# Optimization experiments

Measured on AMD Instinct MI355X. Metric: run time of the kernel, lower is better.

The kernel has to match this reference:

```python
import math
import jax, jax.numpy as jnp
import numpy as np

RMS_EPS = 1.1920929e-07  # torch.finfo(float32).eps used by F.rms_norm default

def _rms_norm(x):
    return x * jax.lax.rsqrt(jnp.mean(jnp.square(x), axis=-1, keepdims=True) + RMS_EPS)

def _rope(x, cos, sin):
    # x: [B,T,H,D]; cos/sin: [T, D//2]
    d = x.shape[-1] // 2
    x1, x2 = x[..., :d], x[..., d:]
    c = cos[None, :, None, :]
    s = sin[None, :, None, :]
    return jnp.concatenate([x1 * c + x2 * s, -x1 * s + x2 * c], axis=-1).astype(x.dtype)

def setup_inputs():
    key = jax.random.key(0)
    ks = jax.random.split(key, 8)
    B, T, C, H, D = 2, 2048, 2048, 16, 128
    x = jax.random.normal(ks[0], (B, T, C), dtype=jnp.float32)
    # real RoPE tables for [T, D//2]
    half = D // 2
    inv_freq = 1.0 / (10000.0 ** (np.arange(half, dtype=np.float32) / half))
    ang = np.outer(np.arange(T, dtype=np.float32), inv_freq)
    cos = jnp.asarray(np.cos(ang), dtype=jnp.float32)
    sin = jnp.asarray(np.sin(ang), dtype=jnp.float32)
    s = 0.02
    Wq = jax.random.normal(ks[1], (C, H * D), dtype=jnp.float32) * s
    Wk = jax.random.normal(ks[2], (C, H * D), dtype=jnp.float32) * s
    Wv = jax.random.normal(ks[3], (C, H * D), dtype=jnp.float32) * s
    Wo = jax.random.normal(ks[4], (C, C), dtype=jnp.float32) * s
    fgate_w = jax.random.normal(ks[5], (C, H), dtype=jnp.float32) * s
    fgate_b = jnp.zeros((H,), dtype=jnp.float32)
    weight_lambda = jax.random.normal(ks[6], (C, H), dtype=jnp.float32) * s
    return dict(x=x, cos=cos, sin=sin, Wq=Wq, Wk=Wk, Wv=Wv, Wo=Wo,
                fgate_w=fgate_w, fgate_b=fgate_b, weight_lambda=weight_lambda,
                window_size=1024)

def reference(x, cos, sin, Wq, Wk, Wv, Wo, fgate_w, fgate_b, weight_lambda, window_size):
    B, T, C = x.shape
    H = fgate_w.shape[1]
    D = Wq.shape[1] // H
    sm_scale = 1.0 / math.sqrt(D)
    # QKV projections (bias=False)
    q = (x @ Wq).reshape(B, T, H, D)
    k = (x @ Wk).reshape(B, T, H, D)
    v = (x @ Wv).reshape(B, T, H, D)
    # RoPE then parameter-free RMSNorm on q,k
    q = _rms_norm(_rope(q, cos, sin))
    k = _rms_norm(_rope(k, cos, sin))
    # [B,H,T,D]
    q = q.transpose(0, 2, 1, 3)
    k = k.transpose(0, 2, 1, 3)
    v = v.transpose(0, 2, 1, 3)
    # forgetting gate: log f_t per (B,H,T)
    lam = jax.nn.elu((x @ weight_lambda).astype(jnp.float32)) + 1.0          # [B,T,H]
    logit = (x @ fgate_w + fgate_b) * lam                                    # [B,T,H]
    log_fgate = (jax.nn.log_sigmoid(logit) / (lam + 0.001)).transpose(0, 2, 1)  # [B,H,T]
    cumF = jnp.cumsum(log_fgate, axis=-1)                                    # [B,H,T]
    # forgetting flash attention, dense reference: bias_ij = cumF_i - cumF_j
    scores = jnp.einsum('bhqd,bhkd->bhqk', q.astype(jnp.float32), k.astype(jnp.float32)) * sm_scale
    scores = scores + cumF[..., :, None] - cumF[..., None, :]
    i = jnp.arange(T)[:, None]
    j = jnp.arange(T)[None, :]
    allowed = (j <= i) & (i - j < window_size)  # causal + sliding window
    scores = jnp.where(allowed, scores, -jnp.inf)
    attn = jax.nn.softmax(scores, axis=-1)
    y = jnp.einsum('bhqk,bhkd->bhqd', attn, v.astype(jnp.float32)).astype(x.dtype)
    y = y.transpose(0, 2, 1, 3).reshape(B, T, C)
    return y @ Wo
```

## Files before the change

### kernel.cpp

```cpp
#include <hip/hip_runtime.h>
#include <hip/hip_bf16.h>
#include <stdint.h>

#define T_SEQ 2048
#define CDIM  2048
#define NHEAD 16
#define DHEAD 128
#define BT    4096
#define BHT   32
#define NQKV  6144

typedef __bf16 bf16x8_t __attribute__((ext_vector_type(8)));
typedef float  f32x4_t  __attribute__((ext_vector_type(4)));
typedef unsigned short u16x8_t __attribute__((ext_vector_type(8)));
typedef unsigned short u16x4_t __attribute__((ext_vector_type(4)));

__device__ __forceinline__ unsigned short f2bf(float f){
  unsigned int u = __float_as_uint(f);
  u += 0x7fffu + ((u >> 16) & 1u);
  return (unsigned short)(u >> 16);
}
__device__ __forceinline__ float bf2f(unsigned short h){
  return __uint_as_float(((unsigned int)h) << 16);
}
__device__ __forceinline__ unsigned ldsaddr(const void* p){
  return (unsigned)(size_t)(const __attribute__((address_space(3))) void*)p;
}
__device__ __forceinline__ u16x4_t tr16(unsigned a){
  u16x4_t r;
  asm volatile("ds_read_b64_tr_b16 %0, %1" : "=v"(r) : "v"(a));
  return r;
}

__global__ __launch_bounds__(256) void transpose_all(const float* __restrict__ Wq,
    const float* __restrict__ Wk, const float* __restrict__ Wv,
    const float* __restrict__ Wo, unsigned short* __restrict__ WqkvT,
    unsigned short* __restrict__ WoT){
  __shared__ float tile[32][33];
  const int z = blockIdx.z;
  const float* W = (z==0)?Wq:(z==1)?Wk:(z==2)?Wv:Wo;
  unsigned short* Wt = (z<3) ? (WqkvT + (size_t)z*4194304) : WoT;
  int n0 = blockIdx.x*32, k0 = blockIdx.y*32;
  int tx = threadIdx.x, ty = threadIdx.y;
  #pragma unroll
  for (int i=0;i<32;i+=8)
    tile[ty+i][tx] = W[(size_t)(k0+ty+i)*CDIM + n0 + tx];
  __syncthreads();
  #pragma unroll
  for (int i=0;i<32;i+=8)
    Wt[(size_t)(n0+ty+i)*CDIM + k0 + tx] = f2bf(tile[tx][ty+i]);
}

__global__ __launch_bounds__(256) void build_wgt(const float* __restrict__ fgw,
                                                 const float* __restrict__ wlam,
                                                 float* __restrict__ WgT){
  int idx = blockIdx.x*256 + threadIdx.x;
  int c = idx >> 11, k = idx & 2047;
  const float* W = (c < 16) ? fgw : wlam;
  WgT[idx] = W[k*16 + (c & 15)];
}

#define V3_SYNC() do{ __builtin_amdgcn_sched_barrier(0); \
  __builtin_amdgcn_s_barrier(); \
  asm volatile("s_waitcnt lgkmcnt(0)" ::: "memory"); \
  __builtin_amdgcn_sched_barrier(0); }while(0)

#define V3_TAIL() do{ asm volatile("s_waitcnt vmcnt(3)" ::: "memory"); \
  __builtin_amdgcn_sched_barrier(0); \
  __builtin_amdgcn_s_barrier(); }while(0)

#define V3_MFMA() do{ __builtin_amdgcn_s_setprio(1); \
  _Pragma("unroll") for (int mi=0;mi<4;mi++) \
  _Pragma("unroll") for (int ni=0;ni<4;ni++) \
    acc[mi][ni] = __builtin_amdgcn_mfma_f32_16x16x32_bf16(af[mi], bfr[ni], acc[mi][ni],0,0,0); \
  __builtin_amdgcn_s_setprio(0); }while(0)

#define V3_PHASE(BUF, TIDX) do{ \
  readA(BUF); readB(BUF); \
  { int ts_ = (TIDX)+2; if (ts_ > ntm1) ts_ = ntm1; stage(((BUF)+2)%3, ts_); } \
  V3_SYNC(); V3_MFMA(); V3_TAIL(); }while(0)

template<int MODE>
__global__ __launch_bounds__(512, 2) void gemm_v3(const unsigned short* __restrict__ A,
                                                  const unsigned short* __restrict__ Bt,
                                                  void* __restrict__ Cout,
                                                  int M, int N, int K){
  extern __shared__ unsigned short lds[];
  const int nx = N >> 8;
  const int Mt = M >> 7;
  const int bid = blockIdx.x;
  const int c8 = bid & 7, w = bid >> 3;
  const int mh = Mt >> 1;
  const int mt = (c8 & 1)*mh + (w % mh);
  const int ntc = (c8 >> 1)*(nx >> 2) + (w / mh);
  const int m0 = mt << 7, n0 = ntc << 8;
  const int tid = threadIdx.x, lane = tid & 63, wv = tid >> 6;
  const int wm = wv >> 2, wn = wv & 3;
  const int g = lane >> 4, qi = lane & 15;
  const int ntm1 = (K >> 5) - 1;

  f32x4_t acc[4][4] = {};
  bf16x8_t af[4], bfr[4];

  int goffA, goffB[2];
  { int s = tid; int row = s >> 2; int lg = (s & 3) ^ ((row >> 1) & 3);
    goffA = row*K + lg*8; }
  #pragma unroll
  for (int j=0;j<2;j++){
    int s = j*512 + tid;
    int row = s >> 2;
    int lg = (s & 3) ^ ((row >> 1) & 3);
    goffB[j] = row*K + lg*8;
  }

  auto stage = [&](int buf, int kt){
    const unsigned short* srcA = A + (size_t)m0*K + kt*32;
    const unsigned short* srcB = Bt + (size_t)n0*K + kt*32;
    unsigned short* base = lds + buf*12288;
    __builtin_amdgcn_global_load_lds(
        (const __attribute__((address_space(1))) void*)(srcA + goffA),
        (__attribute__((address_space(3))) void*)(base + tid*8), 16, 0, 0);
    #pragma unroll
    for (int j=0;j<2;j++)
      __builtin_amdgcn_global_load_lds(
        (const __attribute__((address_space(1))) void*)(srcB + goffB[j]),
        (__attribute__((address_space(3))) void*)(base + 4096 + (j*512 + tid)*8), 16, 0, 0);
  };
  auto readA = [&](int buf){
    const unsigned short* base = lds + buf*12288;
    #pragma unroll
    for (int mi=0;mi<4;mi++){
      int row = wm*64 + mi*16 + qi;
      int gs = g ^ ((row >> 1) & 3);
      af[mi] = *reinterpret_cast<const bf16x8_t*>(base + (row*4 + gs)*8);
    }
  };
  auto readB = [&](int buf){
    const unsigned short* base = lds + buf*12288 + 4096;
    #pragma unroll
    for (int ni=0;ni<4;ni++){
      int row = wn*64 + ni*16 + qi;
      int gs = g ^ ((row >> 1) & 3);
      bfr[ni] = *reinterpret_cast<const bf16x8_t*>(base + (row*4 + gs)*8);
    }
  };

  stage(0,0); stage(1,1);
  asm volatile("s_waitcnt vmcnt(3)" ::: "memory");
  __builtin_amdgcn_sched_barrier(0);
  __builtin_amdgcn_s_barrier();

  for (int it=0; it<21; ++it){
    const int t3 = it*3;
    V3_PHASE(0, t3+0);
    V3_PHASE(1, t3+1);
    V3_PHASE(2, t3+2);
  }
  V3_PHASE(0, 63);
  asm volatile("s_waitcnt vmcnt(0)" ::: "memory");

  #pragma unroll
  for (int mi=0;mi<4;mi++){
    #pragma unroll
    for (int ni=0;ni<4;ni++){
      #pragma unroll
      for (int r=0;r<4;r++){
        int mm = m0 + wm*64 + mi*16 + 4*g + r;
        int nn = n0 + wn*64 + ni*16 + qi;
        float v = acc[mi][ni][r];
        if (MODE == 2){
          ((float*)Cout)[(size_t)mm*N + nn] = v;
        } else {
          int bb2 = mm >> 11, t = mm & (T_SEQ-1);
          int which = nn >> 11;
          int hh = (nn >> 7) & 15, d = nn & (DHEAD-1);
          ((unsigned short*)Cout)[(size_t)which*8388608 +
              (((size_t)bb2*NHEAD + hh)*T_SEQ + t)*DHEAD + d] = f2bf(v);
        }
      }
    }
  }
}

#define GROWS 4
__global__ __launch_bounds__(256) void gates_kernel(const float* __restrict__ x,
    const float* __restrict__ WgT, const float* __restrict__ fgb,
    float* __restrict__ lfg, unsigned short* __restrict__ xb){
  __shared__ float xs[GROWS*2048];
  __shared__ float part[GROWS*32*8];
  const int r0 = blockIdx.x*GROWS;
  const int tid = threadIdx.x;
  const float* xp = x + (size_t)r0*CDIM;
  #pragma unroll
  for (int i=0;i<GROWS*2048/(256*4); i++){
    int e = (i*256+tid)*4;
    *(float4*)(xs+e) = *(const float4*)(xp+e);
  }
  __syncthreads();
  #pragma unroll
  for (int i=0;i<GROWS*2048/(256*8); i++){
    int e = (i*256+tid)*8;
    u16x8_t ob;
    #pragma unroll
    for (int j=0;j<8;j++) ob[j] = f2bf(xs[e+j]);
    *reinterpret_cast<u16x8_t*>(xb + (size_t)r0*CDIM + e) = ob;
  }
  const int c = tid & 31, kseg = tid >> 5;
  const float* wp = WgT + c*2048 + kseg*256;
  const float* xq = xs + kseg*256;
  f32x4_t acc[GROWS] = {};
  for (int kk=0; kk<64; kk++){
    f32x4_t wv = *(const f32x4_t*)(wp + kk*4);
    #pragma unroll
    for (int r=0;r<GROWS;r++){
      f32x4_t xv = *(const f32x4_t*)(xq + r*2048 + kk*4);
      acc[r] += xv*wv;
    }
  }
  #pragma unroll
  for (int r=0;r<GROWS;r++)
    part[(r*32 + c)*8 + kseg] = acc[r][0]+acc[r][1]+acc[r][2]+acc[r][3];
  __syncthreads();
  if (tid < GROWS*32){
    const int r = tid >> 5, c2 = tid & 31;
    const float* pp = part + (r*32+c2)*8;
    float s = pp[0]+pp[1]+pp[2]+pp[3]+pp[4]+pp[5]+pp[6]+pp[7];
    float other = __shfl_xor(s, 16, 64);
    if (c2 < 16){
      float df = s, dl = other;
      float lam = (dl > 0.f) ? (dl + 1.f) : __expf(dl);
      float logit = (df + fgb[c2]) * lam;
      float ls = fminf(logit, 0.f) - log1pf(__expf(-fabsf(logit)));
      float lf = ls / (lam + 0.001f);
      int row = r0 + r;
      int b = row >> 11, t = row & (T_SEQ-1);
      lfg[((size_t)b*NHEAD + c2)*T_SEQ + t] = lf;
    }
  }
}

__global__ __launch_bounds__(256) void cumsum_kernel(const float* __restrict__ lfg,
                                                     float* __restrict__ cumF){
  __shared__ float sums[256];
  const int bh = blockIdx.x;
  const float* in = lfg + (size_t)bh*T_SEQ;
  float* out = cumF + (size_t)bh*T_SEQ;
  const int tid = threadIdx.x;
  float4 a = *(const float4*)(in + tid*8);
  float4 b = *(const float4*)(in + tid*8 + 4);
  float v[8] = {a.x,a.y,a.z,a.w,b.x,b.y,b.z,b.w};
  float run = 0.f;
  #pragma unroll
  for (int e=0;e<8;e++) run += v[e];
  sums[tid] = run;
  __syncthreads();
  for (int off=1; off<256; off<<=1){
    float y = (tid >= off) ? sums[tid-off] : 0.f;
    __syncthreads();
    sums[tid] += y;
    __syncthreads();
  }
  float acc = sums[tid] - run;
  float o[8];
  #pragma unroll
  for (int e=0;e<8;e++){ acc += v[e]; o[e] = acc; }
  *(float4*)(out + tid*8)     = make_float4(o[0],o[1],o[2],o[3]);
  *(float4*)(out + tid*8 + 4) = make_float4(o[4],o[5],o[6],o[7]);
}

__global__ __launch_bounds__(256) void rope_rms(unsigned short* __restrict__ Kh,
    const float* __restrict__ cosT, const float* __restrict__ sinT){
  const int tid = threadIdx.x, lane = tid & 63, wv = tid >> 6;
  const int row = blockIdx.x*4 + wv;
  const int t = row & (T_SEQ-1);
  unsigned short* xp = Kh + (size_t)row*DHEAD;
  float x1 = bf2f(xp[lane]);
  float x2 = bf2f(xp[lane+64]);
  float c = cosT[t*64 + lane];
  float s = sinT[t*64 + lane];
  float o1 = x1*c + x2*s;
  float o2 = x2*c - x1*s;
  float ss = o1*o1 + o2*o2;
  #pragma unroll
  for (int off=1; off<64; off<<=1) ss += __shfl_xor(ss, off, 64);
  float scale = rsqrtf(ss*(1.f/128.f) + 1.1920929e-07f);
  xp[lane]    = f2bf(o1*scale);
  xp[lane+64] = f2bf(o2*scale);
}

__global__ __launch_bounds__(256, 2) void attn_kernel(const unsigned short* __restrict__ Qh,
    const unsigned short* __restrict__ Kh, const unsigned short* __restrict__ Vh,
    const float* __restrict__ cumF, unsigned short* __restrict__ Y,
    const int* __restrict__ winp, const float* __restrict__ cosT,
    const float* __restrict__ sinT){
  __shared__ unsigned short smem[32768];
  const int dlin = blockIdx.y*16 + blockIdx.x;
  const int c8 = dlin & 7, klin = dlin >> 3;
  const int bh = c8 + 8*(klin >> 4);
  const int q0b = (klin & 15)*128;
  const int b = bh >> 4, h = bh & 15;
  const int tid = threadIdx.x, lane = tid & 63, wv = tid >> 6;
  const int g = lane >> 4, qi = lane & 15;
  const int win = *winp;
  const unsigned short* Qp = Qh + (size_t)bh*T_SEQ*DHEAD;
  const unsigned short* Kp = Kh + (size_t)bh*T_SEQ*DHEAD;
  const unsigned short* Vp = Vh + (size_t)bh*T_SEQ*DHEAD;
  const float* cF = cumF + (size_t)bh*T_SEQ;
  const int q0w = q0b + wv*32;
  bf16x8_t qf[2][4];
  float cFq[2];
  #pragma unroll
  for (int qb=0;qb<2;qb++){
    const int qg = q0w + qb*16 + qi;
    const int t = qg & (T_SEQ-1);
    cFq[qb] = cF[qg];
    #pragma unroll
    for (int dt=0;dt<4;dt++)
      qf[qb][dt] = *reinterpret_cast<const bf16x8_t*>(Qp + (size_t)qg*DHEAD + dt*32 + g*8);
    float o[4][8];
    float ssum = 0.f;
    #pragma unroll
    for (int dt=0;dt<2;dt++){
      const float* cp = cosT + t*64 + dt*32 + g*8;
      const float* sp = sinT + t*64 + dt*32 + g*8;
      float4 ca = *(const float4*)cp, cb4 = *(const float4*)(cp+4);
      float4 sa = *(const float4*)sp, sb4 = *(const float4*)(sp+4);
      float cc[8] = {ca.x,ca.y,ca.z,ca.w,cb4.x,cb4.y,cb4.z,cb4.w};
      float sv[8] = {sa.x,sa.y,sa.z,sa.w,sb4.x,sb4.y,sb4.z,sb4.w};
      #pragma unroll
      for (int e=0;e<8;e++){
        float x1 = bf2f(((const u16x8_t*)&qf[qb][dt])[0][e]);
        float x2 = bf2f(((const u16x8_t*)&qf[qb][dt+2])[0][e]);
        float o1 = fmaf(x1, cc[e],  x2*sv[e]);
        float o2 = fmaf(x2, cc[e], -x1*sv[e]);
        o[dt][e] = o1; o[dt+2][e] = o2;
        ssum = fmaf(o1, o1, fmaf(o2, o2, ssum));
      }
    }
    ssum += __shfl_xor(ssum, 16, 64);
    ssum += __shfl_xor(ssum, 32, 64);
    float scale = rsqrtf(ssum*(1.f/128.f) + 1.1920929e-07f);
    #pragma unroll
    for (int dt=0;dt<4;dt++){
      u16x8_t w;
      #pragma unroll
      for (int e=0;e<8;e++) w[e] = f2bf(o[dt][e]*scale);
      qf[qb][dt] = *reinterpret_cast<bf16x8_t*>(&w);
    }
  }
  f32x4_t ot[2][8] = {};
  float mrun[2] = {-1e30f, -1e30f}, lrun[2] = {0.f, 0.f};
  const float sm_scale = 0.08838834764831845f;
  int kbeg = q0b - win + 1; if (kbeg < 0) kbeg = 0; kbeg &= ~63;
  const int nt = (q0b + 128 - kbeg) >> 6;

  auto stage = [&](int bi, int k0s){
    unsigned short* Kd = smem + bi*8192;
    unsigned short* Vd = smem + 16384 + bi*8192;
    #pragma unroll
    for (int jj=0;jj<4;jj++){
      int t = (wv*4+jj)*64 + lane;
      int r = t>>4, cc = t&15;
      __builtin_amdgcn_global_load_lds(
        (const __attribute__((address_space(1))) void*)(Kp + (size_t)(k0s+r)*DHEAD + ((cc ^ (r&7))*8)),
        (__attribute__((address_space(3))) void*)(Kd + t*8), 16, 0, 0);
      int dd = t>>7, kq = (t>>3)&15, rr = (t>>1)&3, hb = t&1;
      __builtin_amdgcn_global_load_lds(
        (const __attribute__((address_space(1))) void*)(Vp + (size_t)(k0s + kq*4 + rr)*DHEAD + dd*16 + hb*8),
        (__attribute__((address_space(3))) void*)(Vd + t*8), 16, 0, 0);
    }
  };

  stage(0, kbeg);
  for (int it=0; it<nt; ++it){
    const int k0 = kbeg + it*64;
    const int cur = it & 1;
    __syncthreads();
    if (it+1 < nt) stage(cur^1, k0+64);
    if (k0 <= q0w+31 && (k0 + 63) >= (q0w - win + 1)){
      const unsigned short* Kc = smem + cur*8192;
      f32x4_t s[2][4] = {};
      __builtin_amdgcn_s_setprio(1);
      #pragma unroll
      for (int dt=0;dt<4;dt++){
        bf16x8_t kf[4];
        #pragma unroll
        for (int kb=0;kb<4;kb++){
          int row = kb*16 + qi;
          kf[kb] = *reinterpret_cast<const bf16x8_t*>(Kc + row*128 + (((dt*4+g) ^ (row&7))*8));
        }
        #pragma unroll
        for (int kb=0;kb<4;kb++){
          s[0][kb] = __builtin_amdgcn_mfma_f32_16x16x32_bf16(kf[kb], qf[0][dt], s[0][kb], 0,0,0);
          s[1][kb] = __builtin_amdgcn_mfma_f32_16x16x32_bf16(kf[kb], qf[1][dt], s[1][kb], 0,0,0);
        }
      }
      __builtin_amdgcn_s_setprio(0);
      float4 cb[4];
      #pragma unroll
      for (int kb=0;kb<4;kb++) cb[kb] = *(const float4*)(cF + k0 + kb*16 + 4*g);
      u16x8_t pb[2][2];
      #pragma unroll
      for (int qb=0;qb<2;qb++){
        const int qg = q0w + qb*16 + qi;
        float p[16], tmax = -INFINITY;
        #pragma unroll
        for (int kb=0;kb<4;kb++){
          #pragma unroll
          for (int r=0;r<4;r++){
            int key = k0 + kb*16 + 4*g + r;
            float sv = fmaf(s[qb][kb][r], sm_scale, cFq[qb] - ((const float*)&cb[kb])[r]);
            bool ok = (key <= qg) && (qg - key < win);
            p[kb*4+r] = ok ? sv : -INFINITY;
            tmax = fmaxf(tmax, p[kb*4+r]);
          }
        }
        tmax = fmaxf(tmax, __shfl_xor(tmax, 16, 64));
        tmax = fmaxf(tmax, __shfl_xor(tmax, 32, 64));
        float mnew = fmaxf(mrun[qb], tmax);
        float alpha = __expf(mrun[qb] - mnew);
        float tsum = 0.f;
        #pragma unroll
        for (int i2=0;i2<16;i2++){ p[i2] = __expf(p[i2] - mnew); tsum += p[i2]; }
        tsum += __shfl_xor(tsum, 16, 64);
        tsum += __shfl_xor(tsum, 32, 64);
        lrun[qb] = lrun[qb]*alpha + tsum;
        mrun[qb] = mnew;
        #pragma unroll
        for (int dt=0;dt<8;dt++) ot[qb][dt] *= alpha;
        #pragma unroll
        for (int cc=0;cc<2;cc++){
          #pragma unroll
          for (int e=0;e<8;e++)
            pb[qb][cc][e] = f2bf(p[(2*cc + (e>>2))*4 + (e&3)]);
        }
      }
      unsigned vbase = ldsaddr(smem + 16384 + cur*8192) + lane*8;
      #pragma unroll
      for (int cc=0;cc<2;cc++){
        u16x4_t vlo[8], vhi[8];
        #pragma unroll
        for (int dt=0;dt<8;dt++){
          vlo[dt] = tr16(vbase + (unsigned)((dt*16 + 8*cc)*128));
          vhi[dt] = tr16(vbase + (unsigned)((dt*16 + 8*cc + 4)*128));
        }
        asm volatile("s_waitcnt lgkmcnt(0)");
        __builtin_amdgcn_sched_barrier(0);
        __builtin_amdgcn_s_setprio(1);
        #pragma unroll
        for (int dt=0;dt<8;dt++){
          u16x8_t vv = __builtin_shufflevector(vlo[dt], vhi[dt], 0,1,2,3,4,5,6,7);
          bf16x8_t vf = *reinterpret_cast<bf16x8_t*>(&vv);
          ot[0][dt] = __builtin_amdgcn_mfma_f32_16x16x32_bf16(vf, *reinterpret_cast<bf16x8_t*>(&pb[0][cc]), ot[0][dt], 0,0,0);
          ot[1][dt] = __builtin_amdgcn_mfma_f32_16x16x32_bf16(vf, *reinterpret_cast<bf16x8_t*>(&pb[1][cc]), ot[1][dt], 0,0,0);
        }
        __builtin_amdgcn_s_setprio(0);
      }
    }
  }
  __syncthreads();
  float invl[2] = {1.f/lrun[0], 1.f/lrun[1]};
  #pragma unroll
  for (int qb=0;qb<2;qb++){
    int qlocal = wv*32 + qb*16 + qi;
    #pragma unroll
    for (int dt=0;dt<8;dt++){
      int d8 = dt*2 + (g>>1);
      u16x4_t w;
      #pragma unroll
      for (int r=0;r<4;r++) w[r] = f2bf(ot[qb][dt][r]*invl[qb]);
      *reinterpret_cast<u16x4_t*>(smem + qlocal*128 + ((d8 ^ (qlocal&7))*8) + 4*(g&1)) = w;
    }
  }
  __syncthreads();
  #pragma unroll
  for (int i=0;i<8;i++){
    int t = i*256 + tid;
    int row = t>>4, cc = t&15;
    u16x8_t v = *reinterpret_cast<const u16x8_t*>(smem + row*128 + ((cc ^ (row&7))*8));
    *reinterpret_cast<u16x8_t*>(Y + ((size_t)b*T_SEQ + q0b + row)*CDIM + h*DHEAD + cc*8) = v;
  }
}

extern "C" void kernel_launch(void* const* d_in, const int* in_sizes, int n_in,
                              void* d_out, int out_size, void* d_ws, size_t ws_size,
                              hipStream_t stream){
  const float* x    = (const float*)d_in[0];
  const float* cosT = (const float*)d_in[1];
  const float* sinT = (const float*)d_in[2];
  const float* Wq   = (const float*)d_in[3];
  const float* Wk   = (const float*)d_in[4];
  const float* Wv   = (const float*)d_in[5];
  const float* Wo   = (const float*)d_in[6];
  const float* fgw  = (const float*)d_in[7];
  const float* fgb  = (const float*)d_in[8];
  const float* wlam = (const float*)d_in[9];
  const int*   winp = (const int*)d_in[10];

  char* ws = (char*)d_ws;
  unsigned short* xb    = (unsigned short*)(ws + 0);
  unsigned short* WqkvT = (unsigned short*)(ws + 16777216);
  unsigned short* WoT   = (unsigned short*)(ws + 41943040);
  unsigned short* QKVh  = (unsigned short*)(ws + 50331648);
  unsigned short* Qh = QKVh;
  unsigned short* Kh = QKVh + 8388608;
  unsigned short* Vh = QKVh + 16777216;
  unsigned short* Yb  = (unsigned short*)(ws + 100663296);
  float* lfg  = (float*)(ws + 117440512);
  float* cumF = (float*)(ws + 117702656);
  float* WgT  = (float*)(ws + 117964800);

  build_wgt<<<256, 256, 0, stream>>>(fgw, wlam, WgT);
  gates_kernel<<<BT/GROWS, 256, 0, stream>>>(x, WgT, fgb, lfg, xb);
  cumsum_kernel<<<BHT, 256, 0, stream>>>(lfg, cumF);

  transpose_all<<<dim3(64,64,4), dim3(32,8), 0, stream>>>(Wq, Wk, Wv, Wo, WqkvT, WoT);

  hipFuncSetAttribute(reinterpret_cast<const void*>(&gemm_v3<1>),
      hipFuncAttributeMaxDynamicSharedMemorySize, 73728);
  hipFuncSetAttribute(reinterpret_cast<const void*>(&gemm_v3<2>),
      hipFuncAttributeMaxDynamicSharedMemorySize, 73728);

  gemm_v3<1><<<(BT/128)*(NQKV/256), 512, 73728, stream>>>(xb, WqkvT, QKVh, BT, NQKV, CDIM);

  rope_rms<<<BHT*T_SEQ/4, 256, 0, stream>>>(Kh, cosT, sinT);

  attn_kernel<<<dim3(16, BHT), 256, 0, stream>>>(Qh, Kh, Vh, cumF, Yb, winp, cosT, sinT);

  gemm_v3<2><<<(BT/128)*(CDIM/256), 512, 73728, stream>>>(Yb, WoT, d_out, BT, CDIM, CDIM);
}
```

Baseline: 285.7 us.

## Add dedicated 128x128-tile Wo projection GEMM with triple-buffered LDS pipeline

Replaces the generic 128x256, 512-thread GEMM used for the output projection with a specialized 128x128, 256-thread kernel. It uses a triple-buffered global_load_lds pipeline, an XOR-swizzled LDS layout, and an XCD-aware block-to-tile mapping. The output GEMM alone had only 256 blocks, so the smaller tile doubles the block count to 512 and allows three blocks per CU. This should improve occupancy and load balance across CUs, at the cost of less data reuse per tile.

```diff
diff --git a/kernel.cpp b/kernel.cpp
--- a/kernel.cpp
+++ b/kernel.cpp
@@ -177,6 +177,106 @@
           ((unsigned short*)Cout)[(size_t)which*8388608 +
               (((size_t)bb2*NHEAD + hh)*T_SEQ + t)*DHEAD + d] = f2bf(v);
         }
+      }
+    }
+  }
+}
+
+#define WO_TAIL() do{ asm volatile("s_waitcnt vmcnt(4)" ::: "memory"); \
+  __builtin_amdgcn_sched_barrier(0); \
+  __builtin_amdgcn_s_barrier(); }while(0)
+
+#define WO_PHASE(BUF, TIDX) do{ \
+  readA(BUF); readB(BUF); \
+  { int ts_ = (TIDX)+2; if (ts_ > ntm1) ts_ = ntm1; stage(((BUF)+2)%3, ts_); } \
+  V3_SYNC(); V3_MFMA(); WO_TAIL(); }while(0)
+
+__global__ __launch_bounds__(256, 3) void gemm_wo(const unsigned short* __restrict__ A,
+                                                  const unsigned short* __restrict__ Bt,
+                                                  float* __restrict__ Cout,
+                                                  int M, int N, int K){
+  extern __shared__ unsigned short lds[];
+  const int nx = N >> 7;
+  const int Mt = M >> 7;
+  const int bid = blockIdx.x;
+  const int c8 = bid & 7, w = bid >> 3;
+  const int mh = Mt >> 1;
+  const int mt = (c8 & 1)*mh + (w % mh);
+  const int ntc = (c8 >> 1)*(nx >> 2) + (w / mh);
+  const int m0 = mt << 7, n0 = ntc << 7;
+  const int tid = threadIdx.x, lane = tid & 63, wv = tid >> 6;
+  const int wm = wv >> 1, wn = wv & 1;
+  const int g = lane >> 4, qi = lane & 15;
+  const int ntm1 = (K >> 5) - 1;
+
+  f32x4_t acc[4][4] = {};
+  bf16x8_t af[4], bfr[4];
+
+  int goff[4], loff[4];
+  #pragma unroll
+  for (int j=0;j<4;j++){
+    int s = j*256 + tid;
+    int si = s & 511;
+    int row = si >> 2;
+    int lg = (si & 3) ^ ((row >> 1) & 3);
+    goff[j] = row*K + lg*8;
+    loff[j] = (s >= 512 ? 4096 : 0) + si*8;
+  }
+
+  auto stage = [&](int buf, int kt){
+    const unsigned short* srcA = A + (size_t)m0*K + kt*32;
+    const unsigned short* srcB = Bt + (size_t)n0*K + kt*32;
+    unsigned short* base = lds + buf*8192;
+    #pragma unroll
+    for (int j=0;j<4;j++){
+      const unsigned short* src = (j >= 2) ? srcB : srcA;
+      __builtin_amdgcn_global_load_lds(
+        (const __attribute__((address_space(1))) void*)(src + goff[j]),
+        (__attribute__((address_space(3))) void*)(base + loff[j]), 16, 0, 0);
+    }
+  };
+  auto readA = [&](int buf){
+    const unsigned short* base = lds + buf*8192;
+    #pragma unroll
+    for (int mi=0;mi<4;mi++){
+      int row = wm*64 + mi*16 + qi;
+      int gs = g ^ ((row >> 1) & 3);
+      af[mi] = *reinterpret_cast<const bf16x8_t*>(base + (row*4 + gs)*8);
+    }
+  };
+  auto readB = [&](int buf){
+    const unsigned short* base = lds + buf*8192 + 4096;
+    #pragma unroll
+    for (int ni=0;ni<4;ni++){
+      int row = wn*64 + ni*16 + qi;
+      int gs = g ^ ((row >> 1) & 3);
+      bfr[ni] = *reinterpret_cast<const bf16x8_t*>(base + (row*4 + gs)*8);
+    }
+  };
+
+  stage(0,0); stage(1,1);
+  asm volatile("s_waitcnt vmcnt(4)" ::: "memory");
+  __builtin_amdgcn_sched_barrier(0);
+  __builtin_amdgcn_s_barrier();
+
+  for (int it=0; it<21; ++it){
+    const int t3 = it*3;
+    WO_PHASE(0, t3+0);
+    WO_PHASE(1, t3+1);
+    WO_PHASE(2, t3+2);
+  }
+  WO_PHASE(0, 63);
+  asm volatile("s_waitcnt vmcnt(0)" ::: "memory");
+
+  #pragma unroll
+  for (int mi=0;mi<4;mi++){
+    #pragma unroll
+    for (int ni=0;ni<4;ni++){
+      #pragma unroll
+      for (int r=0;r<4;r++){
+        int mm = m0 + wm*64 + mi*16 + 4*g + r;
+        int nn = n0 + wn*64 + ni*16 + qi;
+        Cout[(size_t)mm*N + nn] = acc[mi][ni][r];
       }
     }
   }
@@ -518,8 +618,8 @@
 
   hipFuncSetAttribute(reinterpret_cast<const void*>(&gemm_v3<1>),
       hipFuncAttributeMaxDynamicSharedMemorySize, 73728);
-  hipFuncSetAttribute(reinterpret_cast<const void*>(&gemm_v3<2>),
-      hipFuncAttributeMaxDynamicSharedMemorySize, 73728);
+  hipFuncSetAttribute(reinterpret_cast<const void*>(&gemm_wo),
+      hipFuncAttributeMaxDynamicSharedMemorySize, 49152);
 
   gemm_v3<1><<<(BT/128)*(NQKV/256), 512, 73728, stream>>>(xb, WqkvT, QKVh, BT, NQKV, CDIM);
 
@@ -527,5 +627,5 @@
 
   attn_kernel<<<dim3(16, BHT), 256, 0, stream>>>(Qh, Kh, Vh, cumF, Yb, winp, cosT, sinT);
 
-  gemm_v3<2><<<(BT/128)*(CDIM/256), 512, 73728, stream>>>(Yb, WoT, d_out, BT, CDIM, CDIM);
-}
+  gemm_wo<<<(BT/128)*(CDIM/128), 256, 49152, stream>>>(Yb, WoT, (float*)d_out, BT, CDIM, CDIM);
+}
```

Result: no change. 283.6 us (-0.7%).
